# Kernel optimization log

Measured on AMD Instinct MI355X. Metric: run time of the kernel, lower is better.

The kernel has to match this reference:

```python
import jax, jax.numpy as jnp
import numpy as np

N = 10000
E = 160000
IN_CH, HID, OUT = 14, 128, 4
HEADS = 8
NEG_SLOPE = 0.2


def setup_inputs() -> dict:
    key = jax.random.key(0)
    ks = jax.random.split(key, 16)
    glorot = lambda k, shape: jax.random.normal(k, shape, jnp.float32) * np.sqrt(2.0 / (shape[0] + shape[-1]))
    inp = {
        'x': jax.random.normal(ks[0], (N, IN_CH), jnp.float32),
        'edge_index': jax.random.randint(ks[1], (2, E), 0, N, jnp.int64),
        # layer 1: 14 -> 8 heads x 128, concat
        'W1': glorot(ks[2], (IN_CH, HEADS * HID)),
        'a_src1': glorot(ks[3], (HEADS, HID)),
        'a_dst1': glorot(ks[4], (HEADS, HID)),
        'b1': jnp.zeros((HEADS * HID,), jnp.float32),
        # layer 2: 1024 -> 8 heads x 128, concat
        'W2': glorot(ks[5], (HEADS * HID, HEADS * HID)),
        'a_src2': glorot(ks[6], (HEADS, HID)),
        'a_dst2': glorot(ks[7], (HEADS, HID)),
        'b2': jnp.zeros((HEADS * HID,), jnp.float32),
        # layer 3: 1024 -> 1 head x 4, mean (concat=False)
        'W3': glorot(ks[8], (HEADS * HID, OUT)),
        'a_src3': glorot(ks[9], (1, OUT)),
        'a_dst3': glorot(ks[10], (1, OUT)),
        'b3': jnp.zeros((OUT,), jnp.float32),
    }
    return inp


def gat_conv(x, src, dst, W, a_src, a_dst, b, heads, out_ch, concat):
    n = x.shape[0]
    h = (x @ W).reshape(n, heads, out_ch)                      # [N,H,C]
    al_s = jnp.sum(h * a_src, axis=-1)                         # [N,H]
    al_d = jnp.sum(h * a_dst, axis=-1)                         # [N,H]
    e = al_s[src] + al_d[dst]                                  # [E,H]
    e = jnp.where(e > 0, e, NEG_SLOPE * e)                     # LeakyReLU(0.2)
    # segment softmax over incoming edges of each dst node
    m = jax.ops.segment_max(e, dst, num_segments=n)
    ex = jnp.exp(e - m[dst])
    z = jax.ops.segment_sum(ex, dst, num_segments=n)
    alpha = ex / (z[dst] + 1e-16)                              # [E,H]
    out = jax.ops.segment_sum(h[src] * alpha[:, :, None], dst, num_segments=n)  # [N,H,C]
    out = out.reshape(n, heads * out_ch) if concat else out.mean(axis=1)
    return out + b


def reference(x, edge_index, W1, a_src1, a_dst1, b1, W2, a_src2, a_dst2, b2, W3, a_src3, a_dst3, b3):
    n = x.shape[0]
    # add self-loops (PyG GATConv default)
    loop = jnp.arange(n, dtype=edge_index.dtype)
    src = jnp.concatenate([edge_index[0], loop])
    dst = jnp.concatenate([edge_index[1], loop])
    # dropout layers are identity in eval mode
    h = gat_conv(x, src, dst, W1, a_src1, a_dst1, b1, HEADS, HID, True)
    h = jax.nn.relu(h)
    h = gat_conv(h, src, dst, W2, a_src2, a_dst2, b2, HEADS, HID, True)
    h = jax.nn.relu(h)
    h = gat_conv(h, src, dst, W3, a_src3, a_dst3, b3, 1, OUT, False)
    h = jax.nn.relu(h)
    return h
```

## Files before the change

kernel.cpp:

```cpp
#include <hip/hip_runtime.h>

typedef unsigned short ushort_t;
typedef unsigned int uint32;

#define N_NODES 10000
#define N_EDGES 160000
#define ET (N_NODES + N_EDGES)
#define MPAD 10112
#define HT 1024
#define HEADS 8
#define NEG 0.2f

#define O_FLAG     0
#define O_SRC      256
#define O_DST      (O_SRC + 680192)
#define O_COUNTS   (O_DST + 680192)
#define O_OFFS     (O_COUNTS + 40192)
#define O_CURS     (O_OFFS + 40192)
#define O_SSORT    (O_CURS + 40192)
#define O_ALS      (O_SSORT + 680192)
#define O_ALD      (O_ALS + 320000)
#define O_AL3S     (O_ALD + 320000)
#define O_AL3D     (O_AL3S + 40192)
#define O_H3       (O_AL3D + 40192)
#define O_XF       (O_H3 + 160000)
#define O_W1F      (O_XF + 560128)
#define O_AS1F     (O_W1F + 57344)
#define O_W3F      (O_AS1F + 24576)
#define O_S3F      (O_W3F + 16384)
#define O_W2T      (O_S3F + 768)
#define O_BUFA     (O_W2T + 2097152)
#define O_BUFB     (O_BUFA + 20709376)

__device__ __forceinline__ float bf2f(ushort_t u){ return __uint_as_float(((uint32)u) << 16); }
__device__ __forceinline__ ushort_t f2bf(float f){
    uint32 x = __float_as_uint(f);
    return (ushort_t)((x + 0x7fffu + ((x >> 16) & 1u)) >> 16);
}
__device__ __forceinline__ void unpack2(uint32 u, float& lo, float& hi){
    lo = __uint_as_float(u << 16);
    hi = __uint_as_float(u & 0xffff0000u);
}

typedef __bf16 bf16x8 __attribute__((ext_vector_type(8)));
typedef float  f32x4  __attribute__((ext_vector_type(4)));

typedef const __attribute__((address_space(1))) uint32* gas1_u32;
typedef       __attribute__((address_space(3))) uint32* las3_u32;

__device__ __forceinline__ void gload_lds16(const void* g, void* l){
    __builtin_amdgcn_global_load_lds((gas1_u32)g, (las3_u32)l, 16, 0, 0);
}

__device__ __forceinline__ int probe_f32(const uint32* __restrict__ w){
    int cnt = 0;
    for (int i = 0; i < 256; i++){
        uint32 e = (w[i] >> 7) & 0xffu;
        cnt += (e >= 64u && e <= 160u) ? 1 : 0;
    }
    return (cnt > 200) ? 0 : 1;
}
__device__ __forceinline__ int probe_edge64(const int* __restrict__ ei){
    int nz = 0;
    for (int i = 0; i < 128; i++) nz |= ei[2*i + 1];
    return (nz == 0) ? 1 : 0;
}

struct CvtArgs {
    const void* src[12];
    float*      dst[12];
    int         n[12];
};

__global__ __launch_bounds__(256) void k_setup(CvtArgs a, const void* __restrict__ W2,
                                               const uint32* __restrict__ w1raw,
                                               const int* __restrict__ eiraw,
                                               int* __restrict__ counts,
                                               ushort_t* __restrict__ W2T,
                                               int* __restrict__ flags){
    __shared__ ushort_t tile[32][33];
    int slice = blockIdx.y;
    int tid = threadIdx.x;
    if (slice < 12){
        int n = a.n[slice];
        int base = blockIdx.x * 1024 + tid * 4;
        if (base >= n) return;
        int f32 = probe_f32(w1raw);
        const void* s = a.src[slice];
        float* d = a.dst[slice];
        #pragma unroll
        for (int j = 0; j < 4; j++){
            int i = base + j;
            if (i < n) d[i] = f32 ? ((const float*)s)[i] : bf2f(((const ushort_t*)s)[i]);
        }
    } else if (slice == 12){
        if (blockIdx.x == 10){
            if (tid == 0) flags[0] = probe_edge64(eiraw);
            if (tid == 1) flags[1] = probe_f32(w1raw);
            return;
        }
        if (blockIdx.x < 10){
            int i0 = blockIdx.x * 1024 + tid * 4;
            if (i0 + 3 < N_NODES){
                *(int4*)(counts + i0) = make_int4(0,0,0,0);
            } else {
                for (int j = 0; j < 4; j++) if (i0 + j < N_NODES) counts[i0 + j] = 0;
            }
        }
    } else {
        int f32 = probe_f32(w1raw);
        int bx = blockIdx.x & 31, by = blockIdx.x >> 5;
        int cx = tid & 31;
        int ry = (tid >> 5) * 4;
        #pragma unroll
        for (int r = 0; r < 4; r++){
            size_t idx = (size_t)(by*32 + ry + r)*1024 + bx*32 + cx;
            tile[ry + r][cx] = f32 ? f2bf(((const float*)W2)[idx]) : ((const ushort_t*)W2)[idx];
        }
        __syncthreads();
        #pragma unroll
        for (int r = 0; r < 4; r++)
            W2T[(size_t)(bx*32 + ry + r)*1024 + by*32 + cx] = tile[cx][ry + r];
    }
}

__global__ __launch_bounds__(256) void k_extract_hist(const void* __restrict__ ei, const int* __restrict__ flags,
                                                      int* __restrict__ src, int* __restrict__ dst,
                                                      int* __restrict__ counts){
    int i = blockIdx.x * 256 + threadIdx.x;
    int is64 = flags[0];
    int s = -1, d = -1;
    if (i < N_EDGES){
        if (is64){
            const long long* p = (const long long*)ei;
            s = (int)p[i]; d = (int)p[N_EDGES + i];
        } else {
            const int* p = (const int*)ei;
            s = p[i]; d = p[N_EDGES + i];
        }
    } else if (i < ET){
        s = i - N_EDGES; d = s;
    }
    if (d >= 0){
        src[i] = s; dst[i] = d;
        atomicAdd(&counts[d], 1);
    }
}

__global__ __launch_bounds__(1024) void k_scan(const int* __restrict__ counts, int* __restrict__ offs,
                                               int* __restrict__ cursors, int n){
    __shared__ int wsum[16];
    __shared__ int running_s;
    int tid = threadIdx.x;
    int lane = tid & 63, wid = tid >> 6;
    if (tid == 0) running_s = 0;
    __syncthreads();
    for (int base = 0; base < n; base += 1024){
        int i = base + tid;
        int v = (i < n) ? counts[i] : 0;
        int x = v;
        #pragma unroll
        for (int d = 1; d < 64; d <<= 1){
            int t = __shfl_up(x, d, 64);
            if (lane >= d) x += t;
        }
        if (lane == 63) wsum[wid] = x;
        __syncthreads();
        if (wid == 0 && lane < 16){
            int w = wsum[lane];
            #pragma unroll
            for (int d = 1; d < 16; d <<= 1){
                int t = __shfl_up(w, d, 64);
                if (lane >= d) w += t;
            }
            wsum[lane] = w;
        }
        __syncthreads();
        int wprefix = (wid == 0) ? 0 : wsum[wid - 1];
        int run = running_s;
        int excl = run + wprefix + (x - v);
        if (i < n){ offs[i] = excl; cursors[i] = excl; }
        __syncthreads();
        if (tid == 0) running_s = run + wsum[15];
        __syncthreads();
    }
    if (tid == 0) offs[n] = running_s;
}

__global__ __launch_bounds__(256) void k_scatter(const int* __restrict__ src, const int* __restrict__ dst,
                                                 int* __restrict__ cursors, int* __restrict__ ssort){
    int i = blockIdx.x * 256 + threadIdx.x;
    if (i < ET){
        int pos = atomicAdd(&cursors[dst[i]], 1);
        ssort[pos] = src[i];
    }
}

__global__ __launch_bounds__(256) void k_gemm1f(const float* __restrict__ x, const float* __restrict__ W1,
                                                const float* __restrict__ a_src, const float* __restrict__ a_dst,
                                                ushort_t* __restrict__ h1,
                                                float* __restrict__ alS, float* __restrict__ alD){
    __shared__ float w1s[14 * HT];
    int tid = threadIdx.x;
    for (int i = tid * 4; i < 14 * HT; i += 1024)
        *(float4*)(w1s + i) = *(const float4*)(W1 + i);
    int c0 = tid * 4;
    float4 sv = *(const float4*)(a_src + c0);
    float4 dv = *(const float4*)(a_dst + c0);
    int head = tid >> 5, l32 = tid & 31;
    __syncthreads();
    for (int n = blockIdx.x; n < N_NODES; n += gridDim.x){
        float a0=0.f, a1=0.f, a2=0.f, a3=0.f;
        #pragma unroll
        for (int k = 0; k < 14; k++){
            float xv = x[n*14 + k];
            float4 w = *(const float4*)(w1s + k*HT + c0);
            a0 += xv*w.x; a1 += xv*w.y; a2 += xv*w.z; a3 += xv*w.w;
        }
        uint2 o;
        o.x = (uint32)f2bf(a0) | ((uint32)f2bf(a1) << 16);
        o.y = (uint32)f2bf(a2) | ((uint32)f2bf(a3) << 16);
        *(uint2*)(h1 + (size_t)n*HT + c0) = o;
        float h0,h1v,h2,h3v;
        unpack2(o.x, h0, h1v); unpack2(o.y, h2, h3v);
        float s = h0*sv.x + h1v*sv.y + h2*sv.z + h3v*sv.w;
        float d = h0*dv.x + h1v*dv.y + h2*dv.z + h3v*dv.w;
        #pragma unroll
        for (int of = 16; of; of >>= 1){ s += __shfl_xor(s, of, 32); d += __shfl_xor(d, of, 32); }
        if (l32 == 0){ alS[n*HEADS + head] = s; alD[n*HEADS + head] = d; }
    }
}

__global__ __launch_bounds__(256) void k_gat_agg(const ushort_t* __restrict__ H, const float* __restrict__ alS,
                                                 const float* __restrict__ alD, const int* __restrict__ offs,
                                                 const int* __restrict__ srcs, const float* __restrict__ bias,
                                                 ushort_t* __restrict__ out){
    int tid = threadIdx.x;
    int wv = tid >> 6, lane = tid & 63;
    int n = blockIdx.x * 2 + (wv >> 1);
    int half = wv & 1;
    int beg = offs[n], end = offs[n+1];
    int head = half*4 + (lane >> 4);
    int slot = lane & 15;
    float ad = alD[n*HEADS + head];

    float m = -1e30f, z = 0.f;
    for (int c = beg; c < end; c += 64){
        int cn = min(64, end - c);
        int sreg = (lane < cn) ? srcs[c + lane] : 0;
        for (int p = slot; p < cn; p += 16){
            int s = __shfl(sreg, p, 64);
            float v = alS[s*HEADS + head] + ad;
            v = v > 0.f ? v : NEG*v;
            if (v > m){ z = z*__expf(m - v) + 1.f; m = v; }
            else z += __expf(v - m);
        }
    }
    #pragma unroll
    for (int o = 1; o < 16; o <<= 1){
        float m2 = __shfl_xor(m, o, 64);
        float z2 = __shfl_xor(z, o, 64);
        float nm = fmaxf(m, m2);
        z = z*__expf(m - nm) + z2*__expf(m2 - nm);
        m = nm;
    }
    float inv = 1.f / (z + 1e-16f);

    int ch0 = half*512 + lane*8;
    const ushort_t* Hc = H + ch0;
    float c0=0.f,c1=0.f,c2=0.f,c3=0.f,c4=0.f,c5=0.f,c6=0.f,c7=0.f;
    for (int c = beg; c < end; c += 64){
        int cn = min(64, end - c);
        int sreg = (lane < cn) ? srcs[c + lane] : 0;
        int j = 0;
        for (; j + 4 <= cn; j += 4){
            int s0 = __shfl(sreg, j, 64);
            int s1 = __shfl(sreg, j+1, 64);
            int s2 = __shfl(sreg, j+2, 64);
            int s3 = __shfl(sreg, j+3, 64);
            float e0 = alS[s0*HEADS + head];
            float e1 = alS[s1*HEADS + head];
            float e2 = alS[s2*HEADS + head];
            float e3 = alS[s3*HEADS + head];
            uint4 u0 = *(const uint4*)(Hc + (size_t)s0*HT);
            uint4 u1 = *(const uint4*)(Hc + (size_t)s1*HT);
            uint4 u2 = *(const uint4*)(Hc + (size_t)s2*HT);
            uint4 u3 = *(const uint4*)(Hc + (size_t)s3*HT);
            float v0 = e0 + ad; v0 = v0 > 0.f ? v0 : NEG*v0;
            float v1 = e1 + ad; v1 = v1 > 0.f ? v1 : NEG*v1;
            float v2 = e2 + ad; v2 = v2 > 0.f ? v2 : NEG*v2;
            float v3 = e3 + ad; v3 = v3 > 0.f ? v3 : NEG*v3;
            float w0 = __expf(v0 - m) * inv;
            float w1 = __expf(v1 - m) * inv;
            float w2 = __expf(v2 - m) * inv;
            float w3 = __expf(v3 - m) * inv;
            float f0,f1,f2,f3,f4,f5,f6,f7;
            unpack2(u0.x,f0,f1); unpack2(u0.y,f2,f3); unpack2(u0.z,f4,f5); unpack2(u0.w,f6,f7);
            c0+=w0*f0; c1+=w0*f1; c2+=w0*f2; c3+=w0*f3;
            c4+=w0*f4; c5+=w0*f5; c6+=w0*f6; c7+=w0*f7;
            unpack2(u1.x,f0,f1); unpack2(u1.y,f2,f3); unpack2(u1.z,f4,f5); unpack2(u1.w,f6,f7);
            c0+=w1*f0; c1+=w1*f1; c2+=w1*f2; c3+=w1*f3;
            c4+=w1*f4; c5+=w1*f5; c6+=w1*f6; c7+=w1*f7;
            unpack2(u2.x,f0,f1); unpack2(u2.y,f2,f3); unpack2(u2.z,f4,f5); unpack2(u2.w,f6,f7);
            c0+=w2*f0; c1+=w2*f1; c2+=w2*f2; c3+=w2*f3;
            c4+=w2*f4; c5+=w2*f5; c6+=w2*f6; c7+=w2*f7;
            unpack2(u3.x,f0,f1); unpack2(u3.y,f2,f3); unpack2(u3.z,f4,f5); unpack2(u3.w,f6,f7);
            c0+=w3*f0; c1+=w3*f1; c2+=w3*f2; c3+=w3*f3;
            c4+=w3*f4; c5+=w3*f5; c6+=w3*f6; c7+=w3*f7;
        }
        for (; j < cn; j++){
            int s0 = __shfl(sreg, j, 64);
            uint4 u0 = *(const uint4*)(Hc + (size_t)s0*HT);
            float v0 = alS[s0*HEADS + head] + ad;
            v0 = v0 > 0.f ? v0 : NEG*v0;
            float w0 = __expf(v0 - m) * inv;
            float f0,f1,f2,f3,f4,f5,f6,f7;
            unpack2(u0.x,f0,f1); unpack2(u0.y,f2,f3); unpack2(u0.z,f4,f5); unpack2(u0.w,f6,f7);
            c0+=w0*f0; c1+=w0*f1; c2+=w0*f2; c3+=w0*f3;
            c4+=w0*f4; c5+=w0*f5; c6+=w0*f6; c7+=w0*f7;
        }
    }
    float4 b0 = *(const float4*)(bias + ch0);
    float4 b1 = *(const float4*)(bias + ch0 + 4);
    c0 = fmaxf(c0+b0.x, 0.f); c1 = fmaxf(c1+b0.y, 0.f);
    c2 = fmaxf(c2+b0.z, 0.f); c3 = fmaxf(c3+b0.w, 0.f);
    c4 = fmaxf(c4+b1.x, 0.f); c5 = fmaxf(c5+b1.y, 0.f);
    c6 = fmaxf(c6+b1.z, 0.f); c7 = fmaxf(c7+b1.w, 0.f);
    uint4 o;
    o.x = (uint32)f2bf(c0) | ((uint32)f2bf(c1) << 16);
    o.y = (uint32)f2bf(c2) | ((uint32)f2bf(c3) << 16);
    o.z = (uint32)f2bf(c4) | ((uint32)f2bf(c5) << 16);
    o.w = (uint32)f2bf(c6) | ((uint32)f2bf(c7) << 16);
    *(uint4*)(out + (size_t)n*HT + ch0) = o;
}

__global__ __launch_bounds__(256) void k_gemm2(const ushort_t* __restrict__ A, const ushort_t* __restrict__ BT,
                                               ushort_t* __restrict__ C,
                                               const float* __restrict__ aS, const float* __restrict__ aD,
                                               float* __restrict__ alS, float* __restrict__ alD){
    __shared__ ushort_t lA[128*32];
    __shared__ ushort_t lB[128*32];
    __shared__ float reds[2][64][2];
    int L = blockIdx.x;
    int xcd = L & 7;
    int wi  = L >> 3;
    int bm  = xcd * 10 + (wi >> 3);
    int bn  = wi & 7;
    if (bm >= 79) return;
    int tid = threadIdx.x;
    int lane = tid & 63;
    int wave = tid >> 6;
    int wm = (wave & 1) * 64, wn = (wave >> 1) * 64;
    int lm = lane & 15, kg = lane >> 4;
    int sw = (lm >> 1) & 3;
    f32x4 acc[4][4];
    #pragma unroll
    for (int i = 0; i < 4; i++)
        #pragma unroll
        for (int j = 0; j < 4; j++) acc[i][j] = (f32x4)0.0f;

    const int K = 1024;
    int rowA0 = bm * 128, rowB0 = bn * 128;
    for (int k0 = 0; k0 < K; k0 += 32){
        #pragma unroll
        for (int it = 0; it < 2; ++it){
            int s = tid + it*256;
            int r = s >> 2, p = s & 3;
            int qlog = p ^ ((r >> 1) & 3);
            gload_lds16(A  + (size_t)(rowA0 + r)*K + k0 + qlog*8, lA + s*8);
            gload_lds16(BT + (size_t)(rowB0 + r)*K + k0 + qlog*8, lB + s*8);
        }
        __syncthreads();
        bf16x8 af[4], bfr[4];
        int kp = (kg ^ sw) * 8;
        #pragma unroll
        for (int mt = 0; mt < 4; mt++) af[mt]  = *(const bf16x8*)(lA + (wm + mt*16 + lm)*32 + kp);
        #pragma unroll
        for (int nt = 0; nt < 4; nt++) bfr[nt] = *(const bf16x8*)(lB + (wn + nt*16 + lm)*32 + kp);
        #pragma unroll
        for (int mt = 0; mt < 4; mt++)
            #pragma unroll
            for (int nt = 0; nt < 4; nt++)
                acc[mt][nt] = __builtin_amdgcn_mfma_f32_16x16x32_bf16(af[mt], bfr[nt], acc[mt][nt], 0, 0, 0);
        __syncthreads();
    }
    #pragma unroll
    for (int mt = 0; mt < 4; mt++){
        int row_base = bm*128 + wm + mt*16 + kg*4;
        #pragma unroll
        for (int nt = 0; nt < 4; nt++){
            int col = bn*128 + wn + nt*16 + lm;
            #pragma unroll
            for (int r = 0; r < 4; r++){
                int row = row_base + r;
                if (row < N_NODES) C[(size_t)row*HT + col] = f2bf(acc[mt][nt][r]);
            }
        }
    }
    float as_l[4], ad_l[4];
    #pragma unroll
    for (int nt = 0; nt < 4; nt++){
        as_l[nt] = aS[bn*128 + wn + nt*16 + lm];
        ad_l[nt] = aD[bn*128 + wn + nt*16 + lm];
    }
    float psA[4][4], pdA[4][4];
    #pragma unroll
    for (int mt = 0; mt < 4; mt++){
        #pragma unroll
        for (int r = 0; r < 4; r++){
            float ps = acc[mt][0][r]*as_l[0] + acc[mt][1][r]*as_l[1]
                     + acc[mt][2][r]*as_l[2] + acc[mt][3][r]*as_l[3];
            float pd = acc[mt][0][r]*ad_l[0] + acc[mt][1][r]*ad_l[1]
                     + acc[mt][2][r]*ad_l[2] + acc[mt][3][r]*ad_l[3];
            #pragma unroll
            for (int o = 1; o < 16; o <<= 1){ ps += __shfl_xor(ps, o, 64); pd += __shfl_xor(pd, o, 64); }
            psA[mt][r] = ps; pdA[mt][r] = pd;
            if (wn == 64 && lm == 0){
                int rl = mt*16 + kg*4 + r;
                reds[wm >> 6][rl][0] = ps;
                reds[wm >> 6][rl][1] = pd;
            }
        }
    }
    __syncthreads();
    if (wn == 0 && lm == 0){
        #pragma unroll
        for (int mt = 0; mt < 4; mt++){
            #pragma unroll
            for (int r = 0; r < 4; r++){
                int rl = mt*16 + kg*4 + r;
                int row = bm*128 + wm + rl;
                if (row < N_NODES){
                    alS[row*HEADS + bn] = psA[mt][r] + reds[wm >> 6][rl][0];
                    alD[row*HEADS + bn] = pdA[mt][r] + reds[wm >> 6][rl][1];
                }
            }
        }
    }
}

__global__ __launch_bounds__(256) void k_gemm3(const ushort_t* __restrict__ A, const float* __restrict__ W3,
                                               const float* __restrict__ s3,
                                               float* __restrict__ h3, float* __restrict__ al3s, float* __restrict__ al3d){
    int tid = threadIdx.x;
    int lane = tid & 63, wave = tid >> 6;
    int n = blockIdx.x * 4 + wave;
    if (n >= N_NODES) return;
    float4 w3r[16];
    #pragma unroll
    for (int j = 0; j < 16; j++) w3r[j] = ((const float4*)W3)[lane*16 + j];
    const uint4* ap = (const uint4*)(A + (size_t)n*HT + lane*16);
    uint4 u0 = ap[0], u1 = ap[1];
    uint32 uu[8] = {u0.x,u0.y,u0.z,u0.w,u1.x,u1.y,u1.z,u1.w};
    float acc0=0.f, acc1=0.f, acc2=0.f, acc3=0.f;
    #pragma unroll
    for (int p = 0; p < 8; p++){
        float lo, hi;
        unpack2(uu[p], lo, hi);
        float4 wl = w3r[p*2], wh = w3r[p*2+1];
        acc0 += lo*wl.x + hi*wh.x;
        acc1 += lo*wl.y + hi*wh.y;
        acc2 += lo*wl.z + hi*wh.z;
        acc3 += lo*wl.w + hi*wh.w;
    }
    #pragma unroll
    for (int o = 32; o; o >>= 1){
        acc0 += __shfl_xor(acc0, o, 64); acc1 += __shfl_xor(acc1, o, 64);
        acc2 += __shfl_xor(acc2, o, 64); acc3 += __shfl_xor(acc3, o, 64);
    }
    if (lane == 0){
        *(float4*)(h3 + n*4) = make_float4(acc0, acc1, acc2, acc3);
        al3s[n] = acc0*s3[0] + acc1*s3[1] + acc2*s3[2] + acc3*s3[3];
        al3d[n] = acc0*s3[16] + acc1*s3[17] + acc2*s3[18] + acc3*s3[19];
    }
}

__global__ __launch_bounds__(256) void k_gat_agg3(const float* __restrict__ h3, const float* __restrict__ al3s,
                                                  const float* __restrict__ al3d, const int* __restrict__ offs,
                                                  const int* __restrict__ srcs, const float* __restrict__ b3,
                                                  const int* __restrict__ flags, void* __restrict__ out){
    int tid = threadIdx.x;
    int l = tid & 63, wave = tid >> 6;
    int n = blockIdx.x * 4 + wave;
    if (n >= N_NODES) return;
    int beg = offs[n], end = offs[n+1];
    float ad = al3d[n];
    float m = -1e30f;
    for (int e = beg + l; e < end; e += 64){
        float v = al3s[srcs[e]] + ad; v = v > 0.f ? v : NEG*v;
        m = fmaxf(m, v);
    }
    #pragma unroll
    for (int o = 32; o; o >>= 1) m = fmaxf(m, __shfl_xor(m, o, 64));
    float z = 0.f;
    for (int e = beg + l; e < end; e += 64){
        float v = al3s[srcs[e]] + ad; v = v > 0.f ? v : NEG*v;
        z += __expf(v - m);
    }
    #pragma unroll
    for (int o = 32; o; o >>= 1) z += __shfl_xor(z, o, 64);
    float inv = 1.f / (z + 1e-16f);
    float a0=0.f, a1=0.f, a2=0.f, a3=0.f;
    for (int e = beg + l; e < end; e += 64){
        int s = srcs[e];
        float v = al3s[s] + ad; v = v > 0.f ? v : NEG*v;
        float w = __expf(v - m) * inv;
        float4 hv = *(const float4*)(h3 + s*4);
        a0 += w*hv.x; a1 += w*hv.y; a2 += w*hv.z; a3 += w*hv.w;
    }
    #pragma unroll
    for (int o = 32; o; o >>= 1){
        a0 += __shfl_xor(a0, o, 64); a1 += __shfl_xor(a1, o, 64);
        a2 += __shfl_xor(a2, o, 64); a3 += __shfl_xor(a3, o, 64);
    }
    if (l == 0){
        float r0 = fmaxf(a0 + b3[0], 0.f);
        float r1 = fmaxf(a1 + b3[1], 0.f);
        float r2 = fmaxf(a2 + b3[2], 0.f);
        float r3 = fmaxf(a3 + b3[3], 0.f);
        if (flags[1]){
            float* o4 = (float*)out;
            o4[n*4+0]=r0; o4[n*4+1]=r1; o4[n*4+2]=r2; o4[n*4+3]=r3;
        } else {
            ushort_t* o2 = (ushort_t*)out;
            o2[n*4+0]=f2bf(r0); o2[n*4+1]=f2bf(r1); o2[n*4+2]=f2bf(r2); o2[n*4+3]=f2bf(r3);
        }
    }
}

extern "C" void kernel_launch(void* const* d_in, const int* in_sizes, int n_in,
                              void* d_out, int out_size, void* d_ws, size_t ws_size,
                              hipStream_t stream){
    const void* x   = d_in[0];
    const void* ei  = d_in[1];
    const void* W1  = d_in[2];
    const void* as1 = d_in[3];
    const void* ad1 = d_in[4];
    const void* b1  = d_in[5];
    const void* W2  = d_in[6];
    const void* as2 = d_in[7];
    const void* ad2 = d_in[8];
    const void* b2  = d_in[9];
    const void* W3  = d_in[10];
    const void* as3 = d_in[11];
    const void* ad3 = d_in[12];
    const void* b3  = d_in[13];

    char* ws = (char*)d_ws;
    int* flags     = (int*)(ws + O_FLAG);
    int* srcA      = (int*)(ws + O_SRC);
    int* dstA      = (int*)(ws + O_DST);
    int* counts    = (int*)(ws + O_COUNTS);
    int* offs      = (int*)(ws + O_OFFS);
    int* cursors   = (int*)(ws + O_CURS);
    int* ssort     = (int*)(ws + O_SSORT);
    float* alS     = (float*)(ws + O_ALS);
    float* alD     = (float*)(ws + O_ALD);
    float* al3s    = (float*)(ws + O_AL3S);
    float* al3d    = (float*)(ws + O_AL3D);
    float* h3      = (float*)(ws + O_H3);
    float* xF      = (float*)(ws + O_XF);
    float* W1F     = (float*)(ws + O_W1F);
    float* wvecF   = (float*)(ws + O_AS1F);
    float* W3F     = (float*)(ws + O_W3F);
    float* s3F     = (float*)(ws + O_S3F);
    ushort_t* W2T  = (ushort_t*)(ws + O_W2T);
    ushort_t* bufA = (ushort_t*)(ws + O_BUFA);
    ushort_t* bufB = (ushort_t*)(ws + O_BUFB);

    const int EB = (ET + 255) / 256;

    CvtArgs ca;
    ca.src[0]=x;   ca.dst[0]=xF;            ca.n[0]=140000;
    ca.src[1]=W1;  ca.dst[1]=W1F;           ca.n[1]=14336;
    ca.src[2]=as1; ca.dst[2]=wvecF+0*1024;  ca.n[2]=1024;
    ca.src[3]=ad1; ca.dst[3]=wvecF+1*1024;  ca.n[3]=1024;
    ca.src[4]=b1;  ca.dst[4]=wvecF+2*1024;  ca.n[4]=1024;
    ca.src[5]=as2; ca.dst[5]=wvecF+3*1024;  ca.n[5]=1024;
    ca.src[6]=ad2; ca.dst[6]=wvecF+4*1024;  ca.n[6]=1024;
    ca.src[7]=b2;  ca.dst[7]=wvecF+5*1024;  ca.n[7]=1024;
    ca.src[8]=W3;  ca.dst[8]=W3F;           ca.n[8]=4096;
    ca.src[9]=as3; ca.dst[9]=s3F+0;         ca.n[9]=4;
    ca.src[10]=ad3; ca.dst[10]=s3F+16;      ca.n[10]=4;
    ca.src[11]=b3;  ca.dst[11]=s3F+32;      ca.n[11]=4;

    k_setup<<<dim3(1024, 14), 256, 0, stream>>>(ca, W2, (const uint32*)W1, (const int*)ei,
                                                counts, W2T, flags);
    k_extract_hist<<<EB, 256, 0, stream>>>(ei, flags, srcA, dstA, counts);
    k_scan<<<1, 1024, 0, stream>>>(counts, offs, cursors, N_NODES);
    k_scatter<<<EB, 256, 0, stream>>>(srcA, dstA, cursors, ssort);

    k_gemm1f<<<512, 256, 0, stream>>>(xF, W1F, wvecF+0*1024, wvecF+1*1024, bufA, alS, alD);
    k_gat_agg<<<5000, 256, 0, stream>>>(bufA, alS, alD, offs, ssort, wvecF+2*1024, bufB);

    k_gemm2<<<640, 256, 0, stream>>>(bufB, W2T, bufA, wvecF+3*1024, wvecF+4*1024, alS, alD);
    k_gat_agg<<<5000, 256, 0, stream>>>(bufA, alS, alD, offs, ssort, wvecF+5*1024, bufB);

    k_gemm3<<<2500, 256, 0, stream>>>(bufB, W3F, s3F, h3, al3s, al3d);
    k_gat_agg3<<<2500, 256, 0, stream>>>(h3, al3s, al3d, offs, ssort, s3F+32, flags, d_out);
}
```

Before: 328.8 us.

## Double-buffer LDS in layer-2 GEMM with K-tile of 64

Reworks the layer-2 bf16 MFMA GEMM main loop to use two LDS buffers, each holding a 64-wide K slice. The next tile's global-to-LDS loads are issued before the MFMAs on the current tile, so load latency overlaps with compute. The K step doubles from 32 to 64, which halves the number of barriers, and the XOR swizzle is widened to eight 16-byte chunks to suit the wider rows. LDS use grows to 64 KB per block, which may reduce occupancy, and the reduction scratch array now aliases the tile buffers.

```diff
diff --git a/kernel.cpp b/kernel.cpp
--- a/kernel.cpp
+++ b/kernel.cpp
@@ -338,9 +338,8 @@
                                                ushort_t* __restrict__ C,
                                                const float* __restrict__ aS, const float* __restrict__ aD,
                                                float* __restrict__ alS, float* __restrict__ alD){
-    __shared__ ushort_t lA[128*32];
-    __shared__ ushort_t lB[128*32];
-    __shared__ float reds[2][64][2];
+    __shared__ ushort_t lbuf[2][2][128*64];
+    float (*reds)[64][2] = (float (*)[64][2])lbuf;
     int L = blockIdx.x;
     int xcd = L & 7;
     int wi  = L >> 3;
@@ -352,7 +351,7 @@
     int wave = tid >> 6;
     int wm = (wave & 1) * 64, wn = (wave >> 1) * 64;
     int lm = lane & 15, kg = lane >> 4;
-    int sw = (lm >> 1) & 3;
+    int c0 = (kg ^ (lm & 7)) * 8;
     f32x4 acc[4][4];
     #pragma unroll
     for (int i = 0; i < 4; i++)
@@ -361,28 +360,50 @@
 
     const int K = 1024;
     int rowA0 = bm * 128, rowB0 = bn * 128;
-    for (int k0 = 0; k0 < K; k0 += 32){
-        #pragma unroll
-        for (int it = 0; it < 2; ++it){
+
+    auto stage = [&](int buf, int k0){
+        #pragma unroll
+        for (int it = 0; it < 4; ++it){
             int s = tid + it*256;
-            int r = s >> 2, p = s & 3;
-            int qlog = p ^ ((r >> 1) & 3);
-            gload_lds16(A  + (size_t)(rowA0 + r)*K + k0 + qlog*8, lA + s*8);
-            gload_lds16(BT + (size_t)(rowB0 + r)*K + k0 + qlog*8, lB + s*8);
-        }
-        __syncthreads();
-        bf16x8 af[4], bfr[4];
-        int kp = (kg ^ sw) * 8;
-        #pragma unroll
-        for (int mt = 0; mt < 4; mt++) af[mt]  = *(const bf16x8*)(lA + (wm + mt*16 + lm)*32 + kp);
-        #pragma unroll
-        for (int nt = 0; nt < 4; nt++) bfr[nt] = *(const bf16x8*)(lB + (wn + nt*16 + lm)*32 + kp);
+            int r = s >> 3;
+            int q = (s & 7) ^ (r & 7);
+            gload_lds16(A  + (size_t)(rowA0 + r)*K + k0 + q*8, &lbuf[buf][0][s*8]);
+            gload_lds16(BT + (size_t)(rowB0 + r)*K + k0 + q*8, &lbuf[buf][1][s*8]);
+        }
+    };
+
+    stage(0, 0);
+    asm volatile("s_waitcnt vmcnt(0)" ::: "memory");
+    __syncthreads();
+    int cur = 0;
+    for (int k0 = 0; k0 < K; k0 += 64){
+        if (k0 + 64 < K) stage(cur ^ 1, k0 + 64);
+        bf16x8 a0[4], a1[4], b0[4], b1[4];
+        #pragma unroll
+        for (int mt = 0; mt < 4; mt++){
+            const ushort_t* base = &lbuf[cur][0][(wm + mt*16 + lm)*64];
+            a0[mt] = *(const bf16x8*)(base + c0);
+            a1[mt] = *(const bf16x8*)(base + (c0 ^ 32));
+        }
+        #pragma unroll
+        for (int nt = 0; nt < 4; nt++){
+            const ushort_t* base = &lbuf[cur][1][(wn + nt*16 + lm)*64];
+            b0[nt] = *(const bf16x8*)(base + c0);
+            b1[nt] = *(const bf16x8*)(base + (c0 ^ 32));
+        }
         #pragma unroll
         for (int mt = 0; mt < 4; mt++)
             #pragma unroll
             for (int nt = 0; nt < 4; nt++)
-                acc[mt][nt] = __builtin_amdgcn_mfma_f32_16x16x32_bf16(af[mt], bfr[nt], acc[mt][nt], 0, 0, 0);
+                acc[mt][nt] = __builtin_amdgcn_mfma_f32_16x16x32_bf16(a0[mt], b0[nt], acc[mt][nt], 0, 0, 0);
+        #pragma unroll
+        for (int mt = 0; mt < 4; mt++)
+            #pragma unroll
+            for (int nt = 0; nt < 4; nt++)
+                acc[mt][nt] = __builtin_amdgcn_mfma_f32_16x16x32_bf16(a1[mt], b1[nt], acc[mt][nt], 0, 0, 0);
+        asm volatile("s_waitcnt vmcnt(0)" ::: "memory");
         __syncthreads();
+        cur ^= 1;
     }
     #pragma unroll
     for (int mt = 0; mt < 4; mt++){
```

Measured after the change: 318.3 us. 3.2% less time.
